# Kernel tuning notes

Hardware: AMD Instinct MI355X
Metric: run time of the kernel (lower is better)

## Reference

```python
import jax, jax.numpy as jnp
import numpy as np

B, C, P, K, H = 8, 128, 100000, 14, 8  # batch, channels, points, cavities, heads
RADIUS = 0.5


def setup_inputs() -> dict:
    key = jax.random.key(0)
    ks = jax.random.split(key, 11)
    C2 = 2 * C
    s = 0.05
    return {
        "x": jax.random.normal(ks[0], (B, C, P), jnp.float32),
        "points": jax.random.uniform(ks[1], (P, 3), jnp.float32),
        "cavities": jax.random.uniform(ks[2], (K, 3), jnp.float32),
        "w1": jax.random.normal(ks[3], (K, C2, C), jnp.float32) * s,
        "b1": jnp.zeros((K, C2), jnp.float32),
        "w2": jax.random.normal(ks[4], (K, C, C2), jnp.float32) * s,
        "b2": jnp.zeros((K, C), jnp.float32),
        "in_w": jax.random.normal(ks[5], (3 * C, C), jnp.float32) * s,
        "in_b": jnp.zeros((3 * C,), jnp.float32),
        "out_w": jax.random.normal(ks[6], (C, C), jnp.float32) * s,
        "out_b": jnp.zeros((C,), jnp.float32),
    }


def reference(x, points, cavities, w1, b1, w2, b2, in_w, in_b, out_w, out_b):
    dtype = x.dtype
    # ---- cavity pooling: mean of x over points within RADIUS of each cavity ----
    d_cp = jnp.linalg.norm(points[None, :, :] - cavities[:, None, :], axis=-1)  # [K,P]
    mask = (d_cp < RADIUS).astype(dtype)                                        # [K,P]
    counts = mask.sum(axis=1)                                                   # [K]
    sums = jnp.einsum('bcp,kp->bkc', x, mask)                                   # [B,K,C]
    feat = jnp.where(counts[None, :, None] > 0,
                     sums / jnp.maximum(counts, 1.0)[None, :, None],
                     jnp.zeros((), dtype))                                      # [B,K,C]
    # ---- per-cavity MLP: tanh(relu(f @ W1^T + b1) @ W2^T + b2) ----
    h = jax.nn.relu(jnp.einsum('bkc,kdc->bkd', feat, w1) + b1[None])            # [B,K,2C]
    proc = jnp.tanh(jnp.einsum('bkd,kcd->bkc', h, w2) + b2[None])               # [B,K,C]
    # ---- multi-head self-attention over the K=14 cavities (torch MHA semantics) ----
    qkv = jnp.einsum('bkc,ec->bke', proc, in_w) + in_b                          # [B,K,3C]
    q, k_, v = jnp.split(qkv, 3, axis=-1)
    Dh = C // H
    def heads(t):
        return t.reshape(B, K, H, Dh).transpose(0, 2, 1, 3)                     # [B,H,K,Dh]
    qh, kh, vh = heads(q), heads(k_), heads(v)
    scores = jnp.einsum('bhqd,bhkd->bhqk', qh, kh) / np.float32(np.sqrt(Dh))
    attn = jax.nn.softmax(scores, axis=-1)
    oh = jnp.einsum('bhqk,bhkd->bhqd', attn, vh)
    o = oh.transpose(0, 2, 1, 3).reshape(B, K, C)
    attended = jnp.einsum('bkc,oc->bko', o, out_w) + out_b                      # [B,K,C]
    # ---- nearest-cavity gather-add back to every point ----
    d_pk = jnp.linalg.norm(cavities[None, :, :] - points[:, None, :], axis=-1)  # [P,K]
    nearest = jnp.argmin(d_pk, axis=1)                                          # [P]
    att_t = attended.transpose(0, 2, 1)                                         # [B,C,K]
    return x + att_t[:, :, nearest]                                             # [B,C,P]
```

## Files before the change

### kernel.cpp

```cpp
#include <hip/hip_runtime.h>
#include <hip/hip_bf16.h>
#include <math.h>

#define B_ 8
#define C_ 128
#define P_ 100000
#define K_ 14
#define H_ 8
#define DH_ 16
#define C2_ (2*C_)
#define E3_ (3*C_)
#define R2 0.25f

__device__ __forceinline__ int bitsel(unsigned m, int k) {
#if __has_builtin(__builtin_amdgcn_sbfe)
    return __builtin_amdgcn_sbfe((int)m, (unsigned)k, 1u);
#else
    return ((int)(m << (31 - k))) >> 31;
#endif
}

__global__ void geom_kernel(const float* __restrict__ pts,
                            const float* __restrict__ cav,
                            unsigned short* __restrict__ mask,
                            unsigned char* __restrict__ nearest,
                            int* __restrict__ counts) {
    __shared__ float cx[K_], cy[K_], cz[K_];
    __shared__ int sm[K_];
    int tid = threadIdx.x;
    if (tid < K_) {
        cx[tid] = cav[tid*3+0];
        cy[tid] = cav[tid*3+1];
        cz[tid] = cav[tid*3+2];
        sm[tid] = 0;
    }
    __syncthreads();
    int p = blockIdx.x * blockDim.x + tid;
    bool valid = (p < P_);
    int pc = valid ? p : (P_ - 1);
    float px = pts[pc*3+0], py = pts[pc*3+1], pz = pts[pc*3+2];
    unsigned m = 0;
    float best = 1e30f;
    int bi = 0;
    #pragma unroll
    for (int k = 0; k < K_; ++k) {
        float dx = px - cx[k], dy = py - cy[k], dz = pz - cz[k];
        float d2 = dx*dx + dy*dy + dz*dz;
        if (d2 < R2) m |= (1u << k);
        if (d2 < best) { best = d2; bi = k; }
    }
    if (!valid) m = 0;
    if (valid) {
        mask[p] = (unsigned short)m;
        nearest[p] = (unsigned char)bi;
    }
    int lane = tid & 63;
    #pragma unroll
    for (int k = 0; k < K_; ++k) {
        unsigned long long bal = __ballot((m >> k) & 1u);
        if (lane == 0) atomicAdd(&sm[k], (int)__popcll(bal));
    }
    __syncthreads();
    if (tid < K_) atomicAdd(&counts[tid], sm[tid]);
}

__global__ void pool_kernel(const float* __restrict__ x,
                            const unsigned short* __restrict__ mask,
                            float* __restrict__ sums) {
    int row = blockIdx.x;
    int b = row >> 7, c = row & (C_-1);
    int tid = threadIdx.x;
    const float4* xr = (const float4*)(x + (size_t)row * P_);
    const ushort4* mr = (const ushort4*)mask;
    float acc[K_];
    #pragma unroll
    for (int k = 0; k < K_; ++k) acc[k] = 0.f;
    for (int i = tid; i < P_/4; i += 256) {
        float4 xv = xr[i];
        ushort4 mv = mr[i];
        unsigned mx = mv.x, my = mv.y, mz = mv.z, mw = mv.w;
        int bx = __float_as_int(xv.x), by = __float_as_int(xv.y);
        int bz = __float_as_int(xv.z), bw = __float_as_int(xv.w);
        #pragma unroll
        for (int k = 0; k < K_; ++k) {
            acc[k] += __int_as_float(bitsel(mx, k) & bx);
            acc[k] += __int_as_float(bitsel(my, k) & by);
            acc[k] += __int_as_float(bitsel(mz, k) & bz);
            acc[k] += __int_as_float(bitsel(mw, k) & bw);
        }
    }
    int lane = tid & 63, wave = tid >> 6;
    #pragma unroll
    for (int k = 0; k < K_; ++k) {
        float v = acc[k];
        #pragma unroll
        for (int off = 32; off > 0; off >>= 1) v += __shfl_down(v, off);
        acc[k] = v;
    }
    __shared__ float lsum[4][K_];
    if (lane == 0) {
        #pragma unroll
        for (int k = 0; k < K_; ++k) lsum[wave][k] = acc[k];
    }
    __syncthreads();
    if (tid < K_) {
        float t = lsum[0][tid] + lsum[1][tid] + lsum[2][tid] + lsum[3][tid];
        sums[((size_t)b*K_ + tid)*C_ + c] = t;
    }
}

__global__ void mlp_kernel(const float* __restrict__ sums,
                           const int* __restrict__ counts,
                           const float* __restrict__ w1,
                           const float* __restrict__ b1,
                           const float* __restrict__ w2,
                           const float* __restrict__ b2,
                           const float* __restrict__ in_w,
                           const float* __restrict__ in_b,
                           float* __restrict__ qkv_out) {
    int b = blockIdx.x / K_, k = blockIdx.x % K_;
    int tid = threadIdx.x;
    __shared__ float feat[C_];
    __shared__ float h[C2_];
    __shared__ float pr[C_];
    int cnt = counts[k];
    float inv = (cnt > 0) ? (1.f / (float)cnt) : 0.f;
    if (tid < C_) feat[tid] = sums[((size_t)b*K_ + k)*C_ + tid] * inv;
    __syncthreads();
    {
        const float* w1r = w1 + ((size_t)k*C2_ + tid)*C_;
        float a = b1[k*C2_ + tid];
        #pragma unroll 8
        for (int c = 0; c < C_; ++c) a += feat[c] * w1r[c];
        h[tid] = fmaxf(a, 0.f);
    }
    __syncthreads();
    if (tid < C_) {
        const float* w2r = w2 + ((size_t)k*C_ + tid)*C2_;
        float a = b2[k*C_ + tid];
        #pragma unroll 8
        for (int d = 0; d < C2_; ++d) a += h[d] * w2r[d];
        pr[tid] = tanhf(a);
    }
    __syncthreads();
    for (int e = tid; e < E3_; e += 256) {
        const float* wr = in_w + (size_t)e*C_;
        float a = in_b[e];
        #pragma unroll 8
        for (int c = 0; c < C_; ++c) a += pr[c] * wr[c];
        qkv_out[((size_t)b*K_ + k)*E3_ + e] = a;
    }
}

__global__ void attn_kernel(const float* __restrict__ qkv_in,
                            const float* __restrict__ out_w,
                            const float* __restrict__ out_b,
                            float* __restrict__ att) {
    int b = blockIdx.x;
    int tid = threadIdx.x;
    __shared__ float qkv[K_][E3_];
    __shared__ float ov[K_][C_];
    for (int i = tid; i < K_*E3_; i += 256) qkv[i / E3_][i % E3_] = qkv_in[(size_t)b*K_*E3_ + i];
    __syncthreads();
    if (tid < H_*K_) {
        int hh = tid / K_, q = tid % K_;
        const float* qv = &qkv[q][hh*DH_];
        float sc[K_];
        float mx = -1e30f;
        #pragma unroll
        for (int kk = 0; kk < K_; ++kk) {
            float a = 0.f;
            #pragma unroll
            for (int d = 0; d < DH_; ++d) a += qv[d] * qkv[kk][C_ + hh*DH_ + d];
            a *= 0.25f;
            sc[kk] = a;
            mx = fmaxf(mx, a);
        }
        float ssum = 0.f;
        #pragma unroll
        for (int kk = 0; kk < K_; ++kk) { sc[kk] = __expf(sc[kk] - mx); ssum += sc[kk]; }
        float rinv = 1.f / ssum;
        #pragma unroll
        for (int d = 0; d < DH_; ++d) {
            float a = 0.f;
            #pragma unroll
            for (int kk = 0; kk < K_; ++kk) a += sc[kk] * qkv[kk][2*C_ + hh*DH_ + d];
            ov[q][hh*DH_ + d] = a * rinv;
        }
    }
    __syncthreads();
    for (int i = tid; i < K_*C_; i += 256) {
        int kk = i / C_, o = i % C_;
        const float* wr = out_w + (size_t)o*C_;
        float a = out_b[o];
        #pragma unroll 8
        for (int c = 0; c < C_; ++c) a += ov[kk][c] * wr[c];
        att[((size_t)b*K_ + kk)*C_ + o] = a;
    }
}

__global__ void gather_kernel(const float* __restrict__ x,
                              const float* __restrict__ att,
                              const unsigned char* __restrict__ nearest,
                              float* __restrict__ out) {
    int row = blockIdx.y;
    int b = row >> 7, c = row & (C_-1);
    __shared__ float al[K_];
    if (threadIdx.x < K_) al[threadIdx.x] = att[((size_t)b*K_ + threadIdx.x)*C_ + c];
    __syncthreads();
    const float4* xr = (const float4*)(x + (size_t)row * P_);
    float4* orow = (float4*)(out + (size_t)row * P_);
    const uchar4* nr = (const uchar4*)nearest;
    for (int i = blockIdx.x * blockDim.x + threadIdx.x; i < P_/4; i += 13*256) {
        float4 xv = xr[i];
        uchar4 nv = nr[i];
        float4 o;
        o.x = xv.x + al[nv.x];
        o.y = xv.y + al[nv.y];
        o.z = xv.z + al[nv.z];
        o.w = xv.w + al[nv.w];
        orow[i] = o;
    }
}

extern "C" void kernel_launch(void* const* d_in, const int* in_sizes, int n_in,
                              void* d_out, int out_size, void* d_ws, size_t ws_size,
                              hipStream_t stream) {
    const float* x      = (const float*)d_in[0];
    const float* points = (const float*)d_in[1];
    const float* cav    = (const float*)d_in[2];
    const float* w1     = (const float*)d_in[3];
    const float* b1     = (const float*)d_in[4];
    const float* w2     = (const float*)d_in[5];
    const float* b2     = (const float*)d_in[6];
    const float* in_w   = (const float*)d_in[7];
    const float* in_b   = (const float*)d_in[8];
    const float* out_w  = (const float*)d_in[9];
    const float* out_b  = (const float*)d_in[10];
    float* out = (float*)d_out;

    char* w = (char*)d_ws;
    unsigned short* mask    = (unsigned short*)(w + 0);
    unsigned char*  nearest = (unsigned char*)(w + 200192);
    int*            counts  = (int*)(w + 300288);
    float*          sums    = (float*)(w + 300544);
    float*          qkv     = (float*)(w + 358144);
    float*          att     = (float*)(w + 530432);

    hipMemsetAsync(counts, 0, K_ * sizeof(int), stream);
    geom_kernel<<<(P_ + 255)/256, 256, 0, stream>>>(points, cav, mask, nearest, counts);
    pool_kernel<<<B_*C_, 256, 0, stream>>>(x, mask, sums);
    mlp_kernel<<<B_*K_, 256, 0, stream>>>(sums, counts, w1, b1, w2, b2, in_w, in_b, qkv);
    attn_kernel<<<B_, 256, 0, stream>>>(qkv, out_w, out_b, att);
    gather_kernel<<<dim3(13, B_*C_), 256, 0, stream>>>(x, att, nearest, out);
}
```

Baseline: 352.4 us.

## Use float mask with 4-row FMA pooling and nontemporal output stores

The geometry kernel now writes a K-major float 0/1 mask instead of a packed bitmask. The pooling kernel processes four channel rows per block and accumulates with FMAs, so the bit-extract ALU work is replaced and each mask load is shared across rows. The gather kernel writes its output with nontemporal stores to reduce cache pollution. This adds about 5.6MB of mask traffic, served mostly from cache, and the pool kernel runs with fewer, larger blocks, which reduces latency hiding.

After: 376.4 us. 6.8% more time.

```diff
diff --git a/kernel.cpp b/kernel.cpp
--- a/kernel.cpp
+++ b/kernel.cpp
@@ -12,17 +12,11 @@
 #define E3_ (3*C_)
 #define R2 0.25f
 
-__device__ __forceinline__ int bitsel(unsigned m, int k) {
-#if __has_builtin(__builtin_amdgcn_sbfe)
-    return __builtin_amdgcn_sbfe((int)m, (unsigned)k, 1u);
-#else
-    return ((int)(m << (31 - k))) >> 31;
-#endif
-}
+typedef float f32x4_t __attribute__((ext_vector_type(4)));
 
 __global__ void geom_kernel(const float* __restrict__ pts,
                             const float* __restrict__ cav,
-                            unsigned short* __restrict__ mask,
+                            float* __restrict__ maskf,
                             unsigned char* __restrict__ nearest,
                             int* __restrict__ counts) {
     __shared__ float cx[K_], cy[K_], cz[K_];
@@ -42,70 +36,78 @@
     unsigned m = 0;
     float best = 1e30f;
     int bi = 0;
+    float mv[K_];
     #pragma unroll
     for (int k = 0; k < K_; ++k) {
         float dx = px - cx[k], dy = py - cy[k], dz = pz - cz[k];
         float d2 = dx*dx + dy*dy + dz*dz;
-        if (d2 < R2) m |= (1u << k);
+        bool in = (d2 < R2);
+        mv[k] = in ? 1.0f : 0.0f;
+        if (in) m |= (1u << k);
         if (d2 < best) { best = d2; bi = k; }
     }
-    if (!valid) m = 0;
     if (valid) {
-        mask[p] = (unsigned short)m;
+        #pragma unroll
+        for (int k = 0; k < K_; ++k) maskf[(size_t)k*P_ + p] = mv[k];
         nearest[p] = (unsigned char)bi;
     }
     int lane = tid & 63;
     #pragma unroll
     for (int k = 0; k < K_; ++k) {
-        unsigned long long bal = __ballot((m >> k) & 1u);
+        unsigned long long bal = __ballot(valid && ((m >> k) & 1u));
         if (lane == 0) atomicAdd(&sm[k], (int)__popcll(bal));
     }
     __syncthreads();
     if (tid < K_) atomicAdd(&counts[tid], sm[tid]);
 }
 
-__global__ void pool_kernel(const float* __restrict__ x,
-                            const unsigned short* __restrict__ mask,
-                            float* __restrict__ sums) {
-    int row = blockIdx.x;
-    int b = row >> 7, c = row & (C_-1);
-    int tid = threadIdx.x;
-    const float4* xr = (const float4*)(x + (size_t)row * P_);
-    const ushort4* mr = (const ushort4*)mask;
-    float acc[K_];
-    #pragma unroll
-    for (int k = 0; k < K_; ++k) acc[k] = 0.f;
-    for (int i = tid; i < P_/4; i += 256) {
-        float4 xv = xr[i];
-        ushort4 mv = mr[i];
-        unsigned mx = mv.x, my = mv.y, mz = mv.z, mw = mv.w;
-        int bx = __float_as_int(xv.x), by = __float_as_int(xv.y);
-        int bz = __float_as_int(xv.z), bw = __float_as_int(xv.w);
+__global__ __launch_bounds__(512) void pool_kernel(const float* __restrict__ x,
+                                                   const float* __restrict__ maskf,
+                                                   float* __restrict__ sums) {
+    int r0 = blockIdx.x * 4;
+    int tid = threadIdx.x;
+    const float4* xr0 = (const float4*)(x + (size_t)(r0+0) * P_);
+    const float4* xr1 = (const float4*)(x + (size_t)(r0+1) * P_);
+    const float4* xr2 = (const float4*)(x + (size_t)(r0+2) * P_);
+    const float4* xr3 = (const float4*)(x + (size_t)(r0+3) * P_);
+    const float4* mf4 = (const float4*)maskf;
+    float acc[4][K_];
+    #pragma unroll
+    for (int r = 0; r < 4; ++r)
+        #pragma unroll
+        for (int k = 0; k < K_; ++k) acc[r][k] = 0.f;
+    for (int i = tid; i < P_/4; i += 512) {
+        float4 xv0 = xr0[i], xv1 = xr1[i], xv2 = xr2[i], xv3 = xr3[i];
         #pragma unroll
         for (int k = 0; k < K_; ++k) {
-            acc[k] += __int_as_float(bitsel(mx, k) & bx);
-            acc[k] += __int_as_float(bitsel(my, k) & by);
-            acc[k] += __int_as_float(bitsel(mz, k) & bz);
-            acc[k] += __int_as_float(bitsel(mw, k) & bw);
+            float4 mf = mf4[(size_t)k*(P_/4) + i];
+            acc[0][k] = fmaf(xv0.x, mf.x, fmaf(xv0.y, mf.y, fmaf(xv0.z, mf.z, fmaf(xv0.w, mf.w, acc[0][k]))));
+            acc[1][k] = fmaf(xv1.x, mf.x, fmaf(xv1.y, mf.y, fmaf(xv1.z, mf.z, fmaf(xv1.w, mf.w, acc[1][k]))));
+            acc[2][k] = fmaf(xv2.x, mf.x, fmaf(xv2.y, mf.y, fmaf(xv2.z, mf.z, fmaf(xv2.w, mf.w, acc[2][k]))));
+            acc[3][k] = fmaf(xv3.x, mf.x, fmaf(xv3.y, mf.y, fmaf(xv3.z, mf.z, fmaf(xv3.w, mf.w, acc[3][k]))));
         }
     }
     int lane = tid & 63, wave = tid >> 6;
-    #pragma unroll
-    for (int k = 0; k < K_; ++k) {
-        float v = acc[k];
-        #pragma unroll
-        for (int off = 32; off > 0; off >>= 1) v += __shfl_down(v, off);
-        acc[k] = v;
-    }
-    __shared__ float lsum[4][K_];
-    if (lane == 0) {
-        #pragma unroll
-        for (int k = 0; k < K_; ++k) lsum[wave][k] = acc[k];
-    }
-    __syncthreads();
-    if (tid < K_) {
-        float t = lsum[0][tid] + lsum[1][tid] + lsum[2][tid] + lsum[3][tid];
-        sums[((size_t)b*K_ + tid)*C_ + c] = t;
+    __shared__ float lsum[8][4][K_];
+    #pragma unroll
+    for (int r = 0; r < 4; ++r) {
+        #pragma unroll
+        for (int k = 0; k < K_; ++k) {
+            float v = acc[r][k];
+            #pragma unroll
+            for (int off = 32; off > 0; off >>= 1) v += __shfl_down(v, off);
+            if (lane == 0) lsum[wave][r][k] = v;
+        }
+    }
+    __syncthreads();
+    if (tid < 4*K_) {
+        int r = tid / K_, k = tid % K_;
+        float t = 0.f;
+        #pragma unroll
+        for (int w = 0; w < 8; ++w) t += lsum[w][r][k];
+        int row = r0 + r;
+        int b = row >> 7, c = row & (C_-1);
+        sums[((size_t)b*K_ + k)*C_ + c] = t;
     }
 }
 
@@ -209,17 +211,17 @@
     if (threadIdx.x < K_) al[threadIdx.x] = att[((size_t)b*K_ + threadIdx.x)*C_ + c];
     __syncthreads();
     const float4* xr = (const float4*)(x + (size_t)row * P_);
-    float4* orow = (float4*)(out + (size_t)row * P_);
+    f32x4_t* orow = (f32x4_t*)(out + (size_t)row * P_);
     const uchar4* nr = (const uchar4*)nearest;
     for (int i = blockIdx.x * blockDim.x + threadIdx.x; i < P_/4; i += 13*256) {
         float4 xv = xr[i];
         uchar4 nv = nr[i];
-        float4 o;
+        f32x4_t o;
         o.x = xv.x + al[nv.x];
         o.y = xv.y + al[nv.y];
         o.z = xv.z + al[nv.z];
         o.w = xv.w + al[nv.w];
-        orow[i] = o;
+        __builtin_nontemporal_store(o, &orow[i]);
     }
 }
 
@@ -240,16 +242,16 @@
     float* out = (float*)d_out;
 
     char* w = (char*)d_ws;
-    unsigned short* mask    = (unsigned short*)(w + 0);
-    unsigned char*  nearest = (unsigned char*)(w + 200192);
-    int*            counts  = (int*)(w + 300288);
-    float*          sums    = (float*)(w + 300544);
-    float*          qkv     = (float*)(w + 358144);
-    float*          att     = (float*)(w + 530432);
-
-    hipMemsetAsync(counts, 0, K_ * sizeof(int), stream);
-    geom_kernel<<<(P_ + 255)/256, 256, 0, stream>>>(points, cav, mask, nearest, counts);
-    pool_kernel<<<B_*C_, 256, 0, stream>>>(x, mask, sums);
+    float*          maskf   = (float*)(w + 0);
+    unsigned char*  nearest = (unsigned char*)(w + 5600000);
+    int*            counts  = (int*)(w + 5700096);
+    float*          sums    = (float*)(w + 5700352);
+    float*          qkv     = (float*)(w + 5757696);
+    float*          att     = (float*)(w + 5929728);
+
+    (void)hipMemsetAsync(counts, 0, K_ * sizeof(int), stream);
+    geom_kernel<<<(P_ + 255)/256, 256, 0, stream>>>(points, cav, maskf, nearest, counts);
+    pool_kernel<<<256, 512, 0, stream>>>(x, maskf, sums);
     mlp_kernel<<<B_*K_, 256, 0, stream>>>(sums, counts, w1, b1, w2, b2, in_w, in_b, qkv);
     attn_kernel<<<B_, 256, 0, stream>>>(qkv, out_w, out_b, att);
     gather_kernel<<<dim3(13, B_*C_), 256, 0, stream>>>(x, att, nearest, out);
```
